# Kernel tuning notes

Measured on AMD Instinct MI355X. Metric: run time of the kernel, lower is better.

Reference implementation:

```python
import jax, jax.numpy as jnp
import numpy as np

N_NODES = 50000
N_EDGES = 800000
NODE_IN_DIM = 768
NODE_DIM = 512
OUTPUT_NUM = 97
B, P = 8, 2048


def setup_inputs() -> dict:
    key = jax.random.key(0)
    ks = jax.random.split(key, 10)
    node_features = jax.random.normal(ks[0], (N_NODES, NODE_IN_DIM), jnp.float32)
    edge_features = jax.random.normal(ks[1], (N_EDGES, 32), jnp.float32)
    src = jax.random.randint(ks[2], (N_EDGES,), 0, N_NODES)
    dst = jax.random.randint(ks[3], (N_EDGES,), 0, N_NODES)
    head_ent_nodes = jax.random.randint(ks[4], (B, P), 0, N_NODES)
    tail_ent_nodes = jax.random.randint(ks[5], (B, P), 0, N_NODES)
    # params (xavier-ish scale for weights)
    W1 = jax.random.normal(ks[6], (NODE_IN_DIM, NODE_DIM), jnp.float32) / np.sqrt(NODE_IN_DIM)
    b1 = jax.random.normal(ks[7], (NODE_DIM,), jnp.float32) * 0.01
    Wp = jax.random.normal(ks[8], (2 * NODE_DIM, OUTPUT_NUM), jnp.float32) / np.sqrt(2 * NODE_DIM)
    bp = jax.random.normal(ks[9], (OUTPUT_NUM,), jnp.float32) * 0.01
    return {
        "node_features": node_features, "edge_features": edge_features,
        "W1": W1, "b1": b1, "Wp": Wp, "bp": bp,
        "src": src, "dst": dst,
        "head_ent_nodes": head_ent_nodes, "tail_ent_nodes": tail_ent_nodes,
    }


def reference(node_features, edge_features, W1, b1, Wp, bp, src, dst, head_ent_nodes, tail_ent_nodes):
    n = node_features.shape[0]
    # node_fc: Linear + ReLU
    h = jax.nn.relu(node_features @ W1 + b1)  # [N, D]
    # DGL update_all: message = dst node's own h, mean-reduced at dst.
    # (src is part of the graph but unused by this message function.)
    msg = h[dst]  # [E, D] gather
    agg = jax.ops.segment_sum(msg, dst, num_segments=n)  # [N, D]
    deg = jax.ops.segment_sum(jnp.ones((dst.shape[0],), h.dtype), dst, num_segments=n)  # [N]
    # nodes with no incoming messages keep their old h (DGL UDF semantics)
    h_new = jnp.where((deg > 0)[:, None], agg / jnp.maximum(deg, 1.0)[:, None], h)
    head = h_new[head_ent_nodes]  # [B, P, D]
    tail = h_new[tail_ent_nodes]  # [B, P, D]
    out = jnp.concatenate([head, tail], axis=2) @ Wp + bp  # [B, P, 97]
    return out
```

## Files before the change

kernel.cpp:

```cpp
#include <hip/hip_runtime.h>
#include <hip/hip_bf16.h>
#include <stdint.h>

using bf16x8 = __attribute__((ext_vector_type(8))) short;
using f32x4  = __attribute__((ext_vector_type(4))) float;
typedef float f32x4u __attribute__((ext_vector_type(4), aligned(4)));

#define N_NODES  50000
#define K1       768
#define D1       512
#define NPAIR    16384
#define NOUT     97
#define NOUT_PAD 112
#define MTILES   391
#define NTILES   4
#define NWG      (MTILES * NTILES)
#define WGPX     196
#define KSTEPS   24

__device__ __forceinline__ uint16_t f2bf(float f) {
    uint32_t u = __builtin_bit_cast(uint32_t, f);
    return (uint16_t)((u + 0x7fffu + ((u >> 16) & 1u)) >> 16);
}

__device__ __forceinline__ uint32_t cvt_pk_bf16(float lo, float hi) {
    uint32_t r;
    asm("v_cvt_pk_bf16_f32 %0, %1, %2" : "=v"(r) : "v"(lo), "v"(hi));
    return r;
}

__device__ __forceinline__ void gll16(const void* g, void* l) {
    __builtin_amdgcn_global_load_lds(
        (const __attribute__((address_space(1))) void*)g,
        (__attribute__((address_space(3))) void*)l, 16, 0, 0);
}

__global__ __launch_bounds__(256) void k_convert(const float* __restrict__ W1,
        const float* __restrict__ Wp, uint16_t* __restrict__ W1t, uint16_t* __restrict__ Wpt) {
    __shared__ uint16_t lds[32][34];
    const int t = threadIdx.x;
    const int b = blockIdx.x;
    const int lane = t & 31, rw = t >> 5;
    const int lane16 = t & 15, rw2 = t >> 4;

    if (b < 384) {
        const int kt = b % 24, ct = b / 24;
        const int k0 = kt * 32, c0 = ct * 32;
        #pragma unroll
        for (int j = 0; j < 4; ++j) {
            int k = rw + j * 8;
            lds[lane][k] = f2bf(W1[(size_t)(k0 + k) * D1 + c0 + lane]);
        }
        __syncthreads();
        #pragma unroll
        for (int j = 0; j < 2; ++j) {
            int c = rw2 + j * 16;
            uint32_t v = (uint32_t)lds[c][lane16 * 2] | ((uint32_t)lds[c][lane16 * 2 + 1] << 16);
            *(uint32_t*)&W1t[(size_t)(c0 + c) * K1 + k0 + lane16 * 2] = v;
        }
    } else {
        const int b2 = b - 384;
        const int kt = b2 % 32, ct = b2 / 32;
        const int k0 = kt * 32, c0 = ct * 32;
        #pragma unroll
        for (int j = 0; j < 4; ++j) {
            int k = rw + j * 8;
            float v = (c0 + lane < NOUT) ? Wp[(size_t)(k0 + k) * NOUT + c0 + lane] : 0.f;
            lds[lane][k] = f2bf(v);
        }
        __syncthreads();
        #pragma unroll
        for (int j = 0; j < 2; ++j) {
            int c = rw2 + j * 16;
            if (c0 + c < NOUT_PAD) {
                uint32_t v = (uint32_t)lds[c][lane16 * 2] | ((uint32_t)lds[c][lane16 * 2 + 1] << 16);
                *(uint32_t*)&Wpt[(size_t)(c0 + c) * 1024 + k0 + lane16 * 2] = v;
            }
        }
    }
}

__global__ __launch_bounds__(512) void k_gemm1(const float* __restrict__ A,
        const uint16_t* __restrict__ W1t, const float* __restrict__ bias1,
        uint16_t* __restrict__ H) {
    __shared__ float    lds_a[2 * 4096];
    __shared__ uint16_t lds_b[2 * 4096];

    const int bid = blockIdx.x;
    const int tt = (bid & 7) * WGPX + (bid >> 3);
    if (tt >= NWG) return;
    const int m0 = (tt >> 2) * 128, n0 = (tt & 3) * 128;

    const int t = threadIdx.x, lane = t & 63, w = t >> 6;
    const int wm = w >> 1, wn = w & 1;
    const int cl = lane & 15, kh = lane >> 4;

    const float* aSrc[2];
    #pragma unroll
    for (int i = 0; i < 2; ++i) {
        int r = m0 + i * 64 + (t >> 3);
        if (r >= N_NODES) r = N_NODES - 1;
        aSrc[i] = A + (size_t)r * K1 + (((t & 7) ^ ((t >> 3) & 7)) * 4);
    }
    const uint16_t* bSrc =
        W1t + (size_t)(n0 + (t >> 2)) * K1 + (((t & 3) ^ ((t >> 3) & 3)) * 8);

    float*    aDst = &lds_a[w * 256];
    uint16_t* bDst = &lds_b[w * 512];

    const int q7 = cl & 7;
    const int pa0 = ((2 * kh) ^ q7) * 4, pa1 = ((2 * kh + 1) ^ q7) * 4;
    const int arow0 = (wm * 32 + cl) * 32;
    const int brow0 = (wn * 64 + cl) * 32 + ((kh ^ ((cl >> 1) & 3)) * 8);

    f32x4 acc[2][4];
    const f32x4 z = {0.f, 0.f, 0.f, 0.f};
    #pragma unroll
    for (int m = 0; m < 2; ++m)
        #pragma unroll
        for (int n = 0; n < 4; ++n) acc[m][n] = z;

#define STAGE(BUF) do {                                                        \
    gll16(aSrc[0], aDst + (BUF) * 4096);                                       \
    gll16(aSrc[1], aDst + (BUF) * 4096 + 2048);                                \
    gll16(bSrc,    bDst + (BUF) * 4096);                                       \
    aSrc[0] += 32; aSrc[1] += 32; bSrc += 32;                                  \
    } while (0)

#define COMPUTE(BUF) do {                                                      \
    const float*    la = &lds_a[(BUF) * 4096];                                 \
    const uint16_t* lb = &lds_b[(BUF) * 4096];                                 \
    bf16x8 bfr[4];                                                             \
    _Pragma("unroll")                                                          \
    for (int n = 0; n < 4; ++n)                                                \
        bfr[n] = *(const bf16x8*)&lb[brow0 + n * 512];                         \
    _Pragma("unroll")                                                          \
    for (int m = 0; m < 2; ++m) {                                              \
        f32x4 r0 = *(const f32x4*)&la[arow0 + m * 512 + pa0];                  \
        f32x4 r1 = *(const f32x4*)&la[arow0 + m * 512 + pa1];                  \
        uint32_t uu[4];                                                        \
        uu[0] = cvt_pk_bf16(r0[0], r0[1]);                                     \
        uu[1] = cvt_pk_bf16(r0[2], r0[3]);                                     \
        uu[2] = cvt_pk_bf16(r1[0], r1[1]);                                     \
        uu[3] = cvt_pk_bf16(r1[2], r1[3]);                                     \
        bf16x8 af = *(const bf16x8*)uu;                                        \
        _Pragma("unroll")                                                      \
        for (int n = 0; n < 4; ++n)                                            \
            acc[m][n] = __builtin_amdgcn_mfma_f32_16x16x32_bf16(               \
                            bfr[n], af, acc[m][n], 0, 0, 0);                   \
    }                                                                          \
    } while (0)

    STAGE(0);
    for (int kt = 0; kt < KSTEPS - 1; ++kt) {
        const int cur = kt & 1;
        STAGE(cur ^ 1);
        asm volatile("s_waitcnt vmcnt(3)" ::: "memory");
        __builtin_amdgcn_s_barrier();
        COMPUTE(cur);
        __builtin_amdgcn_sched_barrier(0);
        asm volatile("s_waitcnt lgkmcnt(0)" ::: "memory");
        __builtin_amdgcn_s_barrier();
    }
    asm volatile("s_waitcnt vmcnt(0)" ::: "memory");
    __builtin_amdgcn_s_barrier();
    COMPUTE((KSTEPS - 1) & 1);

#undef STAGE
#undef COMPUTE

    float4 bb[4];
    #pragma unroll
    for (int nf = 0; nf < 4; ++nf)
        bb[nf] = *(const float4*)&bias1[n0 + wn * 64 + nf * 16 + kh * 4];
    #pragma unroll
    for (int mf = 0; mf < 2; ++mf) {
        int row = m0 + wm * 32 + mf * 16 + cl;
        if (row < N_NODES) {
            uint16_t* hp = H + (size_t)row * D1 + n0 + wn * 64 + kh * 4;
            #pragma unroll
            for (int nf = 0; nf < 4; ++nf) {
                float v0 = fmaxf(acc[mf][nf][0] + bb[nf].x, 0.f);
                float v1 = fmaxf(acc[mf][nf][1] + bb[nf].y, 0.f);
                float v2 = fmaxf(acc[mf][nf][2] + bb[nf].z, 0.f);
                float v3 = fmaxf(acc[mf][nf][3] + bb[nf].w, 0.f);
                uint2 pk = { cvt_pk_bf16(v0, v1), cvt_pk_bf16(v2, v3) };
                *(uint2*)(hp + nf * 16) = pk;
            }
        }
    }
}

__global__ __launch_bounds__(256) void k_gemm2(const uint16_t* __restrict__ H,
        const uint16_t* __restrict__ Wpt, const float* __restrict__ bp,
        const int* __restrict__ head, const int* __restrict__ tail,
        float* __restrict__ out) {
    __shared__ uint16_t lds_w[NOUT_PAD][40];
    const int t = threadIdx.x;
    const int lane = t & 63, wave = t >> 6;
    const int cl = lane & 15, kh = lane >> 4;
    const int rowbase = blockIdx.x * 64 + wave * 16;
    const int i_l = rowbase + cl;
    const int nodeH = head[i_l], nodeT = tail[i_l];
    const uint16_t* hH = H + (size_t)nodeH * D1 + kh * 8;
    const uint16_t* hT = H + (size_t)nodeT * D1 + kh * 8;

    f32x4 acc[7];
    const f32x4 z = {0.f, 0.f, 0.f, 0.f};
    #pragma unroll
    for (int n = 0; n < 7; ++n) acc[n] = z;

    const int wrow = t >> 1, whalf = t & 1;
    const uint16_t* wsrc = Wpt + (size_t)wrow * 1024 + whalf * 16;
    uint16_t* wdst = &lds_w[wrow][whalf * 16];

    for (int kb = 0; kb < 32; ++kb) {
        uint4 w0 = {0,0,0,0}, w1 = {0,0,0,0};
        if (t < 224) {
            const uint4* wp4 = (const uint4*)(wsrc + kb * 32);
            w0 = wp4[0]; w1 = wp4[1];
        }
        bf16x8 af = (kb < 16) ? *(const bf16x8*)(hH + kb * 32)
                              : *(const bf16x8*)(hT + (kb - 16) * 32);
        __syncthreads();
        if (t < 224) { ((uint4*)wdst)[0] = w0; ((uint4*)wdst)[1] = w1; }
        __syncthreads();
        #pragma unroll
        for (int n = 0; n < 7; ++n) {
            bf16x8 bfr = *(const bf16x8*)&lds_w[n * 16 + cl][kh * 8];
            acc[n] = __builtin_amdgcn_mfma_f32_16x16x32_bf16(bfr, af, acc[n], 0, 0, 0);
        }
    }

    float* op = out + (size_t)(rowbase + cl) * NOUT;
    #pragma unroll
    for (int n = 0; n < 7; ++n) {
        int cb = n * 16 + kh * 4;
        if (cb + 3 < NOUT) {
            float4 bbv = *(const float4*)&bp[cb];
            f32x4u v = { acc[n][0] + bbv.x, acc[n][1] + bbv.y,
                         acc[n][2] + bbv.z, acc[n][3] + bbv.w };
            *(f32x4u*)(op + cb) = v;
        } else if (cb < NOUT) {
            #pragma unroll
            for (int rr = 0; rr < 4; ++rr)
                if (cb + rr < NOUT) op[cb + rr] = acc[n][rr] + bp[cb + rr];
        }
    }
}

extern "C" void kernel_launch(void* const* d_in, const int* in_sizes, int n_in,
                              void* d_out, int out_size, void* d_ws, size_t ws_size,
                              hipStream_t stream) {
    const float* node_features = (const float*)d_in[0];
    const float* W1   = (const float*)d_in[2];
    const float* b1   = (const float*)d_in[3];
    const float* Wp   = (const float*)d_in[4];
    const float* bp   = (const float*)d_in[5];
    const int* head   = (const int*)d_in[8];
    const int* tail   = (const int*)d_in[9];
    float* out = (float*)d_out;

    char* ws = (char*)d_ws;
    uint16_t* H   = (uint16_t*)ws;
    uint16_t* W1t = (uint16_t*)(ws + (size_t)N_NODES * D1 * 2);
    uint16_t* Wpt = (uint16_t*)(ws + (size_t)N_NODES * D1 * 2 + (size_t)D1 * K1 * 2);

    k_convert<<<512, 256, 0, stream>>>(W1, Wp, W1t, Wpt);

    k_gemm1<<<WGPX * 8, 512, 0, stream>>>(node_features, W1t, b1, H);

    k_gemm2<<<NPAIR / 64, 256, 0, stream>>>(H, Wpt, bp, head, tail, out);
}
```

Measured before the change: 104.7 us.

## Convert A tile to bf16 at staging time via register prefetch pipeline

The A operand (fp32 node features) is now loaded into registers with ordinary global loads, converted to bf16 once, and written to LDS as bf16. Previously the fp32 tiles were copied into LDS directly and every wave reconverted them per MFMA. This halves A's LDS footprint, removes redundant per-wave conversions, and raises the occupancy hint to 6 waves per SIMD. The cost is register-staged loads with manual vmcnt bookkeeping in place of direct global-to-LDS copies, which adds VGPR pressure and makes the waits easier to get wrong.

```diff
diff --git a/kernel.cpp b/kernel.cpp
--- a/kernel.cpp
+++ b/kernel.cpp
@@ -80,11 +80,11 @@
     }
 }
 
-__global__ __launch_bounds__(512) void k_gemm1(const float* __restrict__ A,
+__global__ __launch_bounds__(512, 6) void k_gemm1(const float* __restrict__ A,
         const uint16_t* __restrict__ W1t, const float* __restrict__ bias1,
         uint16_t* __restrict__ H) {
-    __shared__ float    lds_a[2 * 4096];
-    __shared__ uint16_t lds_b[2 * 4096];
+    __shared__ uint16_t lds_a[2][128 * 32];
+    __shared__ uint16_t lds_b[2][128 * 32];
 
     const int bid = blockIdx.x;
     const int tt = (bid & 7) * WGPX + (bid >> 3);
@@ -95,23 +95,14 @@
     const int wm = w >> 1, wn = w & 1;
     const int cl = lane & 15, kh = lane >> 4;
 
-    const float* aSrc[2];
-    #pragma unroll
-    for (int i = 0; i < 2; ++i) {
-        int r = m0 + i * 64 + (t >> 3);
-        if (r >= N_NODES) r = N_NODES - 1;
-        aSrc[i] = A + (size_t)r * K1 + (((t & 7) ^ ((t >> 3) & 7)) * 4);
-    }
+    int arow_g = m0 + (t >> 2); if (arow_g >= N_NODES) arow_g = N_NODES - 1;
+    const float* aSrc = A + (size_t)arow_g * K1 + (t & 3) * 8;
+    const int aWrOff = (t >> 2) * 32 + (((t & 3) ^ ((t >> 3) & 3)) * 8);
+
     const uint16_t* bSrc =
         W1t + (size_t)(n0 + (t >> 2)) * K1 + (((t & 3) ^ ((t >> 3) & 3)) * 8);
 
-    float*    aDst = &lds_a[w * 256];
-    uint16_t* bDst = &lds_b[w * 512];
-
-    const int q7 = cl & 7;
-    const int pa0 = ((2 * kh) ^ q7) * 4, pa1 = ((2 * kh + 1) ^ q7) * 4;
-    const int arow0 = (wm * 32 + cl) * 32;
-    const int brow0 = (wn * 64 + cl) * 32 + ((kh ^ ((cl >> 1) & 3)) * 8);
+    const int fo = (kh ^ ((cl >> 1) & 3)) * 8;
 
     f32x4 acc[2][4];
     const f32x4 z = {0.f, 0.f, 0.f, 0.f};
@@ -120,53 +111,73 @@
         #pragma unroll
         for (int n = 0; n < 4; ++n) acc[m][n] = z;
 
-#define STAGE(BUF) do {                                                        \
-    gll16(aSrc[0], aDst + (BUF) * 4096);                                       \
-    gll16(aSrc[1], aDst + (BUF) * 4096 + 2048);                                \
-    gll16(bSrc,    bDst + (BUF) * 4096);                                       \
-    aSrc[0] += 32; aSrc[1] += 32; bSrc += 32;                                  \
+    float4 rA0, rA1;
+
+#define WRITE_A(BUF, R0, R1) do {                                              \
+    uint32_t u0_ = cvt_pk_bf16((R0).x, (R0).y);                                \
+    uint32_t u1_ = cvt_pk_bf16((R0).z, (R0).w);                                \
+    uint32_t u2_ = cvt_pk_bf16((R1).x, (R1).y);                                \
+    uint32_t u3_ = cvt_pk_bf16((R1).z, (R1).w);                                \
+    uint4 v_ = {u0_, u1_, u2_, u3_};                                           \
+    *(uint4*)&lds_a[BUF][aWrOff] = v_;                                         \
     } while (0)
 
 #define COMPUTE(BUF) do {                                                      \
-    const float*    la = &lds_a[(BUF) * 4096];                                 \
-    const uint16_t* lb = &lds_b[(BUF) * 4096];                                 \
-    bf16x8 bfr[4];                                                             \
+    const uint16_t* la_ = &lds_a[BUF][0];                                      \
+    const uint16_t* lb_ = &lds_b[BUF][0];                                      \
+    bf16x8 af_[2], bq_[4];                                                     \
     _Pragma("unroll")                                                          \
-    for (int n = 0; n < 4; ++n)                                                \
-        bfr[n] = *(const bf16x8*)&lb[brow0 + n * 512];                         \
+    for (int nf = 0; nf < 4; ++nf)                                             \
+        bq_[nf] = *(const bf16x8*)&lb_[(wn * 64 + nf * 16 + cl) * 32 + fo];    \
     _Pragma("unroll")                                                          \
-    for (int m = 0; m < 2; ++m) {                                              \
-        f32x4 r0 = *(const f32x4*)&la[arow0 + m * 512 + pa0];                  \
-        f32x4 r1 = *(const f32x4*)&la[arow0 + m * 512 + pa1];                  \
-        uint32_t uu[4];                                                        \
-        uu[0] = cvt_pk_bf16(r0[0], r0[1]);                                     \
-        uu[1] = cvt_pk_bf16(r0[2], r0[3]);                                     \
-        uu[2] = cvt_pk_bf16(r1[0], r1[1]);                                     \
-        uu[3] = cvt_pk_bf16(r1[2], r1[3]);                                     \
-        bf16x8 af = *(const bf16x8*)uu;                                        \
+    for (int mf = 0; mf < 2; ++mf)                                             \
+        af_[mf] = *(const bf16x8*)&la_[(wm * 32 + mf * 16 + cl) * 32 + fo];    \
+    _Pragma("unroll")                                                          \
+    for (int mf = 0; mf < 2; ++mf)                                             \
         _Pragma("unroll")                                                      \
-        for (int n = 0; n < 4; ++n)                                            \
-            acc[m][n] = __builtin_amdgcn_mfma_f32_16x16x32_bf16(               \
-                            bfr[n], af, acc[m][n], 0, 0, 0);                   \
-    }                                                                          \
+        for (int nf = 0; nf < 4; ++nf)                                         \
+            acc[mf][nf] = __builtin_amdgcn_mfma_f32_16x16x32_bf16(             \
+                              bq_[nf], af_[mf], acc[mf][nf], 0, 0, 0);         \
     } while (0)
 
-    STAGE(0);
-    for (int kt = 0; kt < KSTEPS - 1; ++kt) {
-        const int cur = kt & 1;
-        STAGE(cur ^ 1);
-        asm volatile("s_waitcnt vmcnt(3)" ::: "memory");
+    gll16(bSrc, &lds_b[0][w * 512]);
+    {
+        float4 t0 = *(const float4*)(aSrc);
+        float4 t1 = *(const float4*)(aSrc + 4);
+        asm volatile("s_waitcnt vmcnt(0)" ::: "memory");
+        WRITE_A(0, t0, t1);
+    }
+    rA0 = *(const float4*)(aSrc + 32);
+    rA1 = *(const float4*)(aSrc + 36);
+
+    for (int kt = 0; kt < 22; ++kt) {
+        const int cur = kt & 1, nxt = cur ^ 1;
+        gll16(bSrc + (kt + 1) * 32, &lds_b[nxt][w * 512]);
+        asm volatile("s_waitcnt vmcnt(1)" ::: "memory");
+        WRITE_A(nxt, rA0, rA1);
+        rA0 = *(const float4*)(aSrc + (kt + 2) * 32);
+        rA1 = *(const float4*)(aSrc + (kt + 2) * 32 + 4);
+        asm volatile("s_waitcnt lgkmcnt(0)" ::: "memory");
         __builtin_amdgcn_s_barrier();
         COMPUTE(cur);
         __builtin_amdgcn_sched_barrier(0);
         asm volatile("s_waitcnt lgkmcnt(0)" ::: "memory");
         __builtin_amdgcn_s_barrier();
     }
+    gll16(bSrc + 23 * 32, &lds_b[1][w * 512]);
+    asm volatile("s_waitcnt vmcnt(1)" ::: "memory");
+    WRITE_A(1, rA0, rA1);
+    asm volatile("s_waitcnt lgkmcnt(0)" ::: "memory");
+    __builtin_amdgcn_s_barrier();
+    COMPUTE(0);
+    __builtin_amdgcn_sched_barrier(0);
+    asm volatile("s_waitcnt lgkmcnt(0)" ::: "memory");
+    __builtin_amdgcn_s_barrier();
     asm volatile("s_waitcnt vmcnt(0)" ::: "memory");
     __builtin_amdgcn_s_barrier();
-    COMPUTE((KSTEPS - 1) & 1);
-
-#undef STAGE
+    COMPUTE(1);
+
+#undef WRITE_A
 #undef COMPUTE
 
     float4 bb[4];
```

After: 99.11 us. 5.4% less time.
